# Optimization experiments

Hardware: AMD Instinct MI355X
Metric: run time of the kernel (lower is better)

The kernel has to match this reference:

```python
import jax, jax.numpy as jnp
import numpy as np
import math

B, T, E, H, HS = 8, 2048, 384, 6, 64

def setup_inputs() -> dict:
    key = jax.random.key(0)
    ks = jax.random.split(key, 5)
    scale = 1.0 / math.sqrt(E)
    return {
        "x": jax.random.normal(ks[0], (B, T, E), dtype=jnp.float32),
        "Wq": jax.random.normal(ks[1], (H, E, HS), dtype=jnp.float32) * scale,
        "Wk": jax.random.normal(ks[2], (H, E, HS), dtype=jnp.float32) * scale,
        "Wv": jax.random.normal(ks[3], (H, E, HS), dtype=jnp.float32) * scale,
        "Wo": jax.random.normal(ks[4], (H, HS, E), dtype=jnp.float32) * (1.0 / math.sqrt(HS)),
    }

def reference(x, Wq, Wk, Wv, Wo):
    # x: [B,T,E]; per-head projections batched over heads.
    q = jnp.einsum('bte,hed->bhtd', x, Wq)  # [B,H,T,HS]
    k = jnp.einsum('bte,hed->bhtd', x, Wk)
    v = jnp.einsum('bte,hed->bhtd', x, Wv)
    scores = jnp.einsum('bhid,bhjd->bhij', q, k)  # [B,H,T,T]
    # Faithful to source: MULTIPLICATIVE tril mask (masked logits become 0, not -inf),
    # then scale by 1/sqrt(head_size), then softmax.
    t = x.shape[1]
    tril = jnp.tril(jnp.ones((t, t), dtype=scores.dtype))
    scores = scores * tril / math.sqrt(HS)
    attn = jax.nn.softmax(scores, axis=-1)
    ctx = jnp.einsum('bhij,bhjd->bhid', attn, v)  # [B,H,T,HS]
    # Per-head output projection to embed dim, summed over heads (source accumulates).
    out = jnp.einsum('bhtd,hde->bte', ctx, Wo)  # [B,T,E]
    return out
```

## Files before the change

### kernel.cpp

```cpp
#include <hip/hip_runtime.h>
#include <math.h>

#define BBATCH 8
#define TSEQ   2048
#define EDIM   384
#define NHEAD  6
#define DHEAD  64
#define NBH    48
#define QTILE  128
#define NQT    16
#define NW1    442368
#define NW2    147456
#define XSZ    6291456
#define KVSZ   6291456
#define NSLOT  40

typedef __attribute__((ext_vector_type(8)))  short bf16x8;
typedef __attribute__((ext_vector_type(16))) float f32x16;
typedef __attribute__((ext_vector_type(2)))  int   i32x2;
typedef unsigned short u16;
typedef unsigned int   u32;

#define MFMA(a, b, c) __builtin_amdgcn_mfma_f32_32x32x16_bf16(a, b, c, 0, 0, 0)

__device__ __forceinline__ u16 f2bf(float f) {
  u32 u = __float_as_uint(f);
  return (u16)((u + 0x7fffu + ((u >> 16) & 1u)) >> 16);
}
__device__ __forceinline__ float bf2f(u16 h) {
  return __uint_as_float(((u32)h) << 16);
}
__device__ __forceinline__ bf16x8 mk8(u32 w0, u32 w1, u32 w2, u32 w3) {
  union { u32 u[4]; bf16x8 v; } t;
  t.u[0] = w0; t.u[1] = w1; t.u[2] = w2; t.u[3] = w3;
  return t.v;
}

__device__ const unsigned char SLOT_QT[NSLOT] = {
  3,4,5,6,7,7,8,8,9,9,10,10,11,11,11,12,12,12,13,13,13,14,14,14,15,15,15,15,
  2,6,10,14, 1,5,9,13, 0,4,8,12};
__device__ const unsigned char SLOT_C[NSLOT] = {
  0,0,0,0,0,1,0,1,0,1,0,1,0,1,2,0,1,2,0,1,2,0,1,2,0,1,2,3,
  0,1,2,3, 0,1,2,3, 0,1,2,3};

__global__ __launch_bounds__(256) void prep_w_k(
    const float* __restrict__ Wq, const float* __restrict__ Wk,
    const float* __restrict__ Wv, const float* __restrict__ Wo,
    u16* __restrict__ wtH, u16* __restrict__ wtL,
    u16* __restrict__ woH, u16* __restrict__ woL) {
  int idx = blockIdx.x * 256 + threadIdx.x;
  if (idx < NW1) {
    int d = idx & 63;
    int q = idx >> 6;
    int e = q % EDIM;
    int ph = q / EDIM;
    const float* W = (ph < 6) ? Wq : (ph < 12) ? Wk : Wv;
    int h = ph % 6;
    float v = W[((size_t)h * EDIM + e) * DHEAD + d];
    u16 hi = f2bf(v);
    size_t o = ((size_t)ph * DHEAD + d) * EDIM + e;
    wtH[o] = hi;
    wtL[o] = f2bf(v - bf2f(hi));
  } else {
    int o = idx - NW1;
    int eo = o % EDIM;
    int hd = o / EDIM;
    float v = Wo[(size_t)hd * EDIM + eo];
    u16 hi = f2bf(v);
    size_t oo = (size_t)eo * EDIM + hd;
    woH[oo] = hi;
    woL[oo] = f2bf(v - bf2f(hi));
  }
}

__global__ __launch_bounds__(256) void splitx_k(
    const float* __restrict__ x, u16* __restrict__ xh, u16* __restrict__ xl) {
  int i = (blockIdx.x * 256 + threadIdx.x) * 8;
  float4 a = *(const float4*)(x + i);
  float4 b = *(const float4*)(x + i + 4);
  u16 h0 = f2bf(a.x), h1 = f2bf(a.y), h2 = f2bf(a.z), h3 = f2bf(a.w);
  u16 h4 = f2bf(b.x), h5 = f2bf(b.y), h6 = f2bf(b.z), h7 = f2bf(b.w);
  uint4 H, L;
  H.x = (u32)h0 | ((u32)h1 << 16); H.y = (u32)h2 | ((u32)h3 << 16);
  H.z = (u32)h4 | ((u32)h5 << 16); H.w = (u32)h6 | ((u32)h7 << 16);
  L.x = (u32)f2bf(a.x - bf2f(h0)) | ((u32)f2bf(a.y - bf2f(h1)) << 16);
  L.y = (u32)f2bf(a.z - bf2f(h2)) | ((u32)f2bf(a.w - bf2f(h3)) << 16);
  L.z = (u32)f2bf(b.x - bf2f(h4)) | ((u32)f2bf(b.y - bf2f(h5)) << 16);
  L.w = (u32)f2bf(b.z - bf2f(h6)) | ((u32)f2bf(b.w - bf2f(h7)) << 16);
  *(uint4*)(xh + i) = H;
  *(uint4*)(xl + i) = L;
}

__global__ __launch_bounds__(256, 2) void proj_k(
    const u16* __restrict__ xh, const u16* __restrict__ xl,
    const u16* __restrict__ wtH, const u16* __restrict__ wtL,
    u16* __restrict__ qh, u16* __restrict__ ql,
    u16* __restrict__ kh, u16* __restrict__ kl,
    u16* __restrict__ vTh, u16* __restrict__ vTl,
    float* __restrict__ psum) {
  __shared__ __align__(16) unsigned char sm[32768];
  const int tid = threadIdx.x;
  const int w = tid >> 6, l = tid & 63, lh = l >> 5, l31 = l & 31;
  const int gid = ((blockIdx.x & 7) * 288) + ((int)blockIdx.x >> 3);
  const int bx = gid / 18, ph = gid % 18;
  const int p = ph / 6, h = ph % 6;
  const int bt0 = bx * 128;
  const u16* __restrict__ wBh = wtH + (size_t)ph * DHEAD * EDIM;
  const u16* __restrict__ wBl = wtL + (size_t)ph * DHEAD * EDIM;

  f32x16 acc0, acc1;
#pragma unroll
  for (int i = 0; i < 16; ++i) { acc0[i] = 0.f; acc1[i] = 0.f; }

  for (int k0 = 0; k0 < EDIM; k0 += 64) {
    __syncthreads();
#pragma unroll
    for (int i = 0; i < 4; ++i) {
      int c = tid + i * 256;
      int r = c >> 3, s = c & 7;
      int off = (r * 128 + s * 16) ^ ((r & 7) << 4);
      size_t g = (size_t)(bt0 + r) * EDIM + k0 + s * 8;
      *(uint4*)(sm + off) = *(const uint4*)(xh + g);
      *(uint4*)(sm + 16384 + off) = *(const uint4*)(xl + g);
    }
    __syncthreads();
    const int arow = 32 * w + l31;
#pragma unroll
    for (int ks = 0; ks < 4; ++ks) {
      int aoff = (arow * 128 + ks * 32 + 16 * lh) ^ ((arow & 7) << 4);
      bf16x8 aH = *(const bf16x8*)(sm + aoff);
      bf16x8 aL = *(const bf16x8*)(sm + 16384 + aoff);
      int eoff = k0 + ks * 16 + 8 * lh;
      size_t b0 = (size_t)l31 * EDIM + eoff;
      size_t b1 = (size_t)(32 + l31) * EDIM + eoff;
      bf16x8 bH0 = *(const bf16x8*)(wBh + b0);
      bf16x8 bL0 = *(const bf16x8*)(wBl + b0);
      bf16x8 bH1 = *(const bf16x8*)(wBh + b1);
      bf16x8 bL1 = *(const bf16x8*)(wBl + b1);
      acc0 = MFMA(aH, bH0, acc0); acc0 = MFMA(aH, bL0, acc0); acc0 = MFMA(aL, bH0, acc0);
      acc1 = MFMA(aH, bH1, acc1); acc1 = MFMA(aH, bL1, acc1); acc1 = MFMA(aL, bH1, acc1);
    }
  }

  const int b = bt0 >> 11, t0b = bt0 & (TSEQ - 1);
  const int bh = b * NHEAD + h;
  const float scale = (p == 0) ? 0.125f : 1.0f;

  if (p < 2) {
    u16* oH = (p == 0) ? qh : kh;
    u16* oL = (p == 0) ? ql : kl;
#pragma unroll
    for (int reg = 0; reg < 16; ++reg) {
      int row = (reg & 3) + 8 * (reg >> 2) + 4 * lh + 32 * w;
      size_t base = ((size_t)bh * TSEQ + t0b + row) * DHEAD;
      float v0 = acc0[reg] * scale, v1 = acc1[reg] * scale;
      u16 h0 = f2bf(v0), h1 = f2bf(v1);
      oH[base + l31] = h0;       oL[base + l31] = f2bf(v0 - bf2f(h0));
      oH[base + 32 + l31] = h1;  oL[base + 32 + l31] = f2bf(v1 - bf2f(h1));
    }
  } else {
    u16* T = (u16*)sm;
#pragma unroll
    for (int half = 0; half < 2; ++half) {
      __syncthreads();
#pragma unroll
      for (int reg = 0; reg < 16; ++reg) {
        int t = (reg & 3) + 8 * (reg >> 2) + 4 * lh + 32 * w;
        float v0 = acc0[reg], v1 = acc1[reg];
        u16 e0, e1;
        if (half == 0) { e0 = f2bf(v0); e1 = f2bf(v1); }
        else {
          u16 a0 = f2bf(v0), a1 = f2bf(v1);
          e0 = f2bf(v0 - bf2f(a0)); e1 = f2bf(v1 - bf2f(a1));
        }
        T[l31 * 132 + t] = e0;
        T[(32 + l31) * 132 + t] = e1;
      }
      __syncthreads();
      u16* dst = half ? vTl : vTh;
#pragma unroll
      for (int i = 0; i < 8; ++i) {
        int c = tid + i * 256;
        int d = c >> 5, s = c & 31;
        uint2 val = *(const uint2*)(T + d * 132 + s * 4);
        *(uint2*)(dst + ((size_t)bh * DHEAD + d) * TSEQ + t0b + s * 4) = val;
      }
    }
    float s0 = 0.f, s1 = 0.f;
#pragma unroll
    for (int reg = 0; reg < 16; ++reg) { s0 += acc0[reg]; s1 += acc1[reg]; }
    s0 += __shfl_xor(s0, 32);
    s1 += __shfl_xor(s1, 32);
    __syncthreads();
    float* ps = (float*)sm;
    if (lh == 0) { ps[w * 64 + l31] = s0; ps[w * 64 + 32 + l31] = s1; }
    __syncthreads();
    if (tid < 64) {
      float t = ps[tid] + ps[64 + tid] + ps[128 + tid] + ps[192 + tid];
      int tile = t0b >> 7;
      psum[((size_t)bh * NQT + tile) * DHEAD + tid] = t;
    }
  }
}

__global__ __launch_bounds__(256, 4) void attn_k(
    const u16* __restrict__ qh, const u16* __restrict__ ql,
    const u16* __restrict__ kh, const u16* __restrict__ kl,
    const u16* __restrict__ vTh, const u16* __restrict__ vTl,
    float* __restrict__ pO, float* __restrict__ pl) {
  __shared__ __align__(16) unsigned char sm[32768];
  const int oKl = 8192, oVh = 16384, oVl = 24576;
  const int tid = threadIdx.x;
  const int w = tid >> 6, l = tid & 63, lh = l >> 5, l31 = l & 31;
  const int gid = ((blockIdx.x & 7) * 240) + ((int)blockIdx.x >> 3);
  const int bh = gid / NSLOT, slot = gid % NSLOT;
  const int qt = SLOT_QT[slot], cch = SLOT_C[slot];
  const int tbeg = cch * 8;
  const int tend = min(cch * 8 + 8, 2 * qt + 2);
  const int t0 = qt * QTILE;
  const size_t kvb = (size_t)bh * TSEQ * DHEAD;

#pragma unroll
  for (int i = 0; i < 4; ++i) {
    int c = tid + i * 256;
    int r = c >> 3, s = c & 7;
    int off = (r * 128 + s * 16) ^ ((r & 7) << 4);
    size_t g = kvb + (size_t)(t0 + r) * DHEAD + s * 8;
    *(uint4*)(sm + off) = *(const uint4*)(qh + g);
    *(uint4*)(sm + 16384 + off) = *(const uint4*)(ql + g);
  }
  __syncthreads();
  bf16x8 qfH[4], qfL[4];
  {
    const int qrow = 32 * w + l31;
#pragma unroll
    for (int ks = 0; ks < 4; ++ks) {
      int off = (qrow * 128 + ks * 32 + 16 * lh) ^ ((qrow & 7) << 4);
      qfH[ks] = *(const bf16x8*)(sm + off);
      qfL[ks] = *(const bf16x8*)(sm + 16384 + off);
    }
  }
  uint4 kpH[2], kpL[2], vpH[2], vpL[2];
#pragma unroll
  for (int i = 0; i < 2; ++i) {
    int c = tid + i * 256;
    int r = c >> 3, s = c & 7;
    int j0 = tbeg * 64;
    kpH[i] = *(const uint4*)(kh + kvb + (size_t)(j0 + r) * DHEAD + s * 8);
    kpL[i] = *(const uint4*)(kl + kvb + (size_t)(j0 + r) * DHEAD + s * 8);
    vpH[i] = *(const uint4*)(vTh + kvb + (size_t)r * TSEQ + j0 + s * 8);
    vpL[i] = *(const uint4*)(vTl + kvb + (size_t)r * TSEQ + j0 + s * 8);
  }
  __syncthreads();

  f32x16 accO0, accO1;
#pragma unroll
  for (int i = 0; i < 16; ++i) { accO0[i] = 0.f; accO1[i] = 0.f; }
  float lrun = 0.f;
  const int qg = t0 + 32 * w + l31;

  for (int jt = tbeg; jt < tend; ++jt) {
#pragma unroll
    for (int i = 0; i < 2; ++i) {
      int c = tid + i * 256;
      int r = c >> 3, s = c & 7;
      int off = (r * 128 + s * 16) ^ ((r & 7) << 4);
      *(uint4*)(sm + off) = kpH[i];
      *(uint4*)(sm + oKl + off) = kpL[i];
      *(uint4*)(sm + oVh + off) = vpH[i];
      *(uint4*)(sm + oVl + off) = vpL[i];
    }
    __syncthreads();
    if (jt + 1 < tend) {
      int j0 = (jt + 1) * 64;
#pragma unroll
      for (int i = 0; i < 2; ++i) {
        int c = tid + i * 256;
        int r = c >> 3, s = c & 7;
        kpH[i] = *(const uint4*)(kh + kvb + (size_t)(j0 + r) * DHEAD + s * 8);
        kpL[i] = *(const uint4*)(kl + kvb + (size_t)(j0 + r) * DHEAD + s * 8);
        vpH[i] = *(const uint4*)(vTh + kvb + (size_t)r * TSEQ + j0 + s * 8);
        vpL[i] = *(const uint4*)(vTl + kvb + (size_t)r * TSEQ + j0 + s * 8);
      }
    }
#pragma unroll
    for (int jh = 0; jh < 2; ++jh) {
      f32x16 accS;
#pragma unroll
      for (int i = 0; i < 16; ++i) accS[i] = 0.f;
      const int krow = jh * 32 + l31;
      const int ksw = (l31 & 7) << 4;
      __builtin_amdgcn_s_setprio(1);
#pragma unroll
      for (int ks = 0; ks < 4; ++ks) {
        int koff = (krow * 128 + ks * 32 + 16 * lh) ^ ksw;
        bf16x8 aH = *(const bf16x8*)(sm + koff);
        bf16x8 aL = *(const bf16x8*)(sm + oKl + koff);
        accS = MFMA(aH, qfH[ks], accS);
        accS = MFMA(aH, qfL[ks], accS);
        accS = MFMA(aL, qfH[ks], accS);
      }
      __builtin_amdgcn_s_setprio(0);
      const int jb = jt * 64 + jh * 32 + 4 * lh;
      float ps = 0.f;
#pragma unroll
      for (int ml = 0; ml < 2; ++ml) {
        int rb = ml * 8;
        u32 hw[4], lw[4];
#pragma unroll
        for (int pr = 0; pr < 4; ++pr) {
          int r0 = rb + 2 * pr;
          int jg0 = jb + (r0 & 3) + 8 * (r0 >> 2);
          float s0 = (jg0 > qg) ? 0.f : accS[r0];
          float s1 = ((jg0 + 1) > qg) ? 0.f : accS[r0 + 1];
          float p0 = __expf(s0), p1 = __expf(s1);
          ps += p0 + p1;
          u16 a0 = f2bf(p0), a1 = f2bf(p1);
          hw[pr] = (u32)a0 | ((u32)a1 << 16);
          lw[pr] = (u32)f2bf(p0 - bf2f(a0)) | ((u32)f2bf(p1 - bf2f(a1)) << 16);
        }
        i32x2 s1 = __builtin_amdgcn_permlane32_swap((int)hw[0], (int)hw[2], false, false);
        i32x2 s2 = __builtin_amdgcn_permlane32_swap((int)hw[1], (int)hw[3], false, false);
        bf16x8 pH = mk8((u32)s1.x, (u32)s2.x, (u32)s1.y, (u32)s2.y);
        i32x2 t1 = __builtin_amdgcn_permlane32_swap((int)lw[0], (int)lw[2], false, false);
        i32x2 t2 = __builtin_amdgcn_permlane32_swap((int)lw[1], (int)lw[3], false, false);
        bf16x8 pL = mk8((u32)t1.x, (u32)t2.x, (u32)t1.y, (u32)t2.y);
        int m = jh * 2 + ml;
        int vo0 = (l31 * 128 + m * 32 + 16 * lh) ^ ksw;
        int vo1 = ((32 + l31) * 128 + m * 32 + 16 * lh) ^ ksw;
        bf16x8 vH0 = *(const bf16x8*)(sm + oVh + vo0);
        bf16x8 vL0 = *(const bf16x8*)(sm + oVl + vo0);
        bf16x8 vH1 = *(const bf16x8*)(sm + oVh + vo1);
        bf16x8 vL1 = *(const bf16x8*)(sm + oVl + vo1);
        __builtin_amdgcn_s_setprio(1);
        accO0 = MFMA(pH, vH0, accO0); accO0 = MFMA(pH, vL0, accO0); accO0 = MFMA(pL, vH0, accO0);
        accO1 = MFMA(pH, vH1, accO1); accO1 = MFMA(pH, vL1, accO1); accO1 = MFMA(pL, vH1, accO1);
        __builtin_amdgcn_s_setprio(0);
      }
      lrun += ps;
    }
    __syncthreads();
  }

  lrun += __shfl_xor(lrun, 32);
  const size_t slotO = ((size_t)bh * NQT + qt);
  if (lh == 0)
    atomicAdd(&pl[slotO * 128 + 32 * w + l31], lrun);
  float* po = pO + slotO * 8192;
#pragma unroll
  for (int reg = 0; reg < 16; ++reg) {
    int r = (reg & 3) + 8 * (reg >> 2) + 4 * lh + 32 * w;
    atomicAdd(&po[r * 64 + l31], accO0[reg]);
    atomicAdd(&po[r * 64 + 32 + l31], accO1[reg]);
  }
}

__global__ __launch_bounds__(256) void combine_k(
    const float* __restrict__ pO, const float* __restrict__ pl,
    const float* __restrict__ psum,
    u16* __restrict__ cxh, u16* __restrict__ cxl) {
  const int bid = blockIdx.x;
  const int bh = bid >> 4, qt = bid & 15;
  const int b = bh / NHEAD, h = bh % NHEAD;
  const int tid = threadIdx.x;
  const int d = tid & 63, rg = tid >> 6;
  float tail = 0.f;
  for (int tt = qt + 1; tt < NQT; ++tt)
    tail += psum[((size_t)bh * NQT + tt) * DHEAD + d];
  const float tcnt = (float)(TSEQ - (qt + 1) * 128);
  const float* po = pO + (size_t)bid * 8192;
  const float* plp = pl + (size_t)bid * 128;
#pragma unroll 4
  for (int k = 0; k < 32; ++k) {
    int r = rg * 32 + k;
    float inv = 1.0f / (plp[r] + tcnt);
    float v = (po[r * 64 + d] + tail) * inv;
    u16 hbits = f2bf(v);
    size_t o = ((size_t)b * TSEQ + qt * 128 + r) * EDIM + h * DHEAD + d;
    cxh[o] = hbits;
    cxl[o] = f2bf(v - bf2f(hbits));
  }
}

__global__ __launch_bounds__(256, 2) void outproj_k(
    const u16* __restrict__ cxh, const u16* __restrict__ cxl,
    const u16* __restrict__ woH, const u16* __restrict__ woL,
    float* __restrict__ out) {
  __shared__ __align__(16) unsigned char sm[32768];
  const int tid = threadIdx.x;
  const int w = tid >> 6, l = tid & 63, lh = l >> 5, l31 = l & 31;
  const int gid = ((blockIdx.x & 7) * 96) + ((int)blockIdx.x >> 3);
  const int bx = gid / 6, ey = gid % 6;
  const int bt0 = bx * 128, e0 = ey * 64;

  f32x16 acc0, acc1;
#pragma unroll
  for (int i = 0; i < 16; ++i) { acc0[i] = 0.f; acc1[i] = 0.f; }

  for (int k0 = 0; k0 < EDIM; k0 += 64) {
    __syncthreads();
#pragma unroll
    for (int i = 0; i < 4; ++i) {
      int c = tid + i * 256;
      int r = c >> 3, s = c & 7;
      int off = (r * 128 + s * 16) ^ ((r & 7) << 4);
      size_t g = (size_t)(bt0 + r) * EDIM + k0 + s * 8;
      *(uint4*)(sm + off) = *(const uint4*)(cxh + g);
      *(uint4*)(sm + 16384 + off) = *(const uint4*)(cxl + g);
    }
    __syncthreads();
    const int arow = 32 * w + l31;
#pragma unroll
    for (int ks = 0; ks < 4; ++ks) {
      int aoff = (arow * 128 + ks * 32 + 16 * lh) ^ ((arow & 7) << 4);
      bf16x8 aH = *(const bf16x8*)(sm + aoff);
      bf16x8 aL = *(const bf16x8*)(sm + 16384 + aoff);
      int hdoff = k0 + ks * 16 + 8 * lh;
      size_t b0 = (size_t)(e0 + l31) * EDIM + hdoff;
      size_t b1 = (size_t)(e0 + 32 + l31) * EDIM + hdoff;
      bf16x8 bH0 = *(const bf16x8*)(woH + b0);
      bf16x8 bL0 = *(const bf16x8*)(woL + b0);
      bf16x8 bH1 = *(const bf16x8*)(woH + b1);
      bf16x8 bL1 = *(const bf16x8*)(woL + b1);
      acc0 = MFMA(aH, bH0, acc0); acc0 = MFMA(aH, bL0, acc0); acc0 = MFMA(aL, bH0, acc0);
      acc1 = MFMA(aH, bH1, acc1); acc1 = MFMA(aH, bL1, acc1); acc1 = MFMA(aL, bH1, acc1);
    }
  }
#pragma unroll
  for (int reg = 0; reg < 16; ++reg) {
    int row = (reg & 3) + 8 * (reg >> 2) + 4 * lh + 32 * w;
    size_t o = (size_t)(bt0 + row) * EDIM + e0;
    out[o + l31] = acc0[reg];
    out[o + 32 + l31] = acc1[reg];
  }
}

extern "C" void kernel_launch(void* const* d_in, const int* in_sizes, int n_in,
                              void* d_out, int out_size, void* d_ws, size_t ws_size,
                              hipStream_t stream) {
  (void)in_sizes; (void)n_in; (void)out_size; (void)ws_size;
  const float* x  = (const float*)d_in[0];
  const float* Wq = (const float*)d_in[1];
  const float* Wk = (const float*)d_in[2];
  const float* Wv = (const float*)d_in[3];
  const float* Wo = (const float*)d_in[4];
  float* out = (float*)d_out;

  u16* qh  = (u16*)d_ws;
  u16* ql  = qh + KVSZ;
  u16* kh  = ql + KVSZ;
  u16* kl  = kh + KVSZ;
  u16* vTh = kl + KVSZ;
  u16* vTl = vTh + KVSZ;
  u16* xh  = vTl + KVSZ;
  u16* xl  = xh + XSZ;
  u16* wtH = xl + XSZ;
  u16* wtL = wtH + NW1;
  u16* woH = wtL + NW1;
  u16* woL = woH + NW2;
  float* psum = (float*)(woL + NW2);
  float* pO   = psum + (size_t)NBH * NQT * DHEAD;
  float* pl   = pO + (size_t)NBH * NQT * 128 * 64;
  u16* cxh = xh;
  u16* cxl = xl;

  hipMemsetAsync(pO, 0, ((size_t)NBH * NQT * 128 * 65) * sizeof(float), stream);
  hipLaunchKernelGGL(prep_w_k, dim3((NW1 + NW2) / 256), dim3(256), 0, stream,
                     Wq, Wk, Wv, Wo, wtH, wtL, woH, woL);
  hipLaunchKernelGGL(splitx_k, dim3(XSZ / 2048), dim3(256), 0, stream, x, xh, xl);
  hipLaunchKernelGGL(proj_k, dim3(2304), dim3(256), 0, stream,
                     xh, xl, wtH, wtL, qh, ql, kh, kl, vTh, vTl, psum);
  hipLaunchKernelGGL(attn_k, dim3(1920), dim3(256), 0, stream,
                     qh, ql, kh, kl, vTh, vTl, pO, pl);
  hipLaunchKernelGGL(combine_k, dim3(NBH * NQT), dim3(256), 0, stream,
                     pO, pl, psum, cxh, cxl);
  hipLaunchKernelGGL(outproj_k, dim3(768), dim3(256), 0, stream,
                     cxh, cxl, woH, woL, out);
}
```

Before: 551.2 us.

## Use single-wave attention blocks reading K/V from global, fuse combine step

The attention kernel is restructured from 256-thread blocks with LDS-staged K/V and split-KV slots into 64-thread single-wave blocks. Each block owns 32 query rows and walks the whole causal key range, loading K and V fragments straight from global memory (relying on cache). The softmax normalisation and masked-tail correction now happen in the epilogue, so the separate combine kernel, the atomics and the memset are removed. The QK accumulation is also split over two accumulators to shorten MFMA dependency chains. The cost is heavier per-wave global/L2 traffic for K/V with no LDS sharing, and causal load imbalance because work is no longer split across KV chunks.

Result: faster. 460.6 us (-16.4%).

```diff
diff --git a/kernel.cpp b/kernel.cpp
--- a/kernel.cpp
+++ b/kernel.cpp
@@ -13,7 +13,6 @@
 #define NW2    147456
 #define XSZ    6291456
 #define KVSZ   6291456
-#define NSLOT  40
 
 typedef __attribute__((ext_vector_type(8)))  short bf16x8;
 typedef __attribute__((ext_vector_type(16))) float f32x16;
@@ -35,13 +34,6 @@
   t.u[0] = w0; t.u[1] = w1; t.u[2] = w2; t.u[3] = w3;
   return t.v;
 }
-
-__device__ const unsigned char SLOT_QT[NSLOT] = {
-  3,4,5,6,7,7,8,8,9,9,10,10,11,11,11,12,12,12,13,13,13,14,14,14,15,15,15,15,
-  2,6,10,14, 1,5,9,13, 0,4,8,12};
-__device__ const unsigned char SLOT_C[NSLOT] = {
-  0,0,0,0,0,1,0,1,0,1,0,1,0,1,2,0,1,2,0,1,2,0,1,2,0,1,2,3,
-  0,1,2,3, 0,1,2,3, 0,1,2,3};
 
 __global__ __launch_bounds__(256) void prep_w_k(
     const float* __restrict__ Wq, const float* __restrict__ Wk,
@@ -203,104 +195,62 @@
   }
 }
 
-__global__ __launch_bounds__(256, 4) void attn_k(
+__global__ __launch_bounds__(64, 3) void attn_k(
     const u16* __restrict__ qh, const u16* __restrict__ ql,
     const u16* __restrict__ kh, const u16* __restrict__ kl,
     const u16* __restrict__ vTh, const u16* __restrict__ vTl,
-    float* __restrict__ pO, float* __restrict__ pl) {
-  __shared__ __align__(16) unsigned char sm[32768];
-  const int oKl = 8192, oVh = 16384, oVl = 24576;
-  const int tid = threadIdx.x;
-  const int w = tid >> 6, l = tid & 63, lh = l >> 5, l31 = l & 31;
-  const int gid = ((blockIdx.x & 7) * 240) + ((int)blockIdx.x >> 3);
-  const int bh = gid / NSLOT, slot = gid % NSLOT;
-  const int qt = SLOT_QT[slot], cch = SLOT_C[slot];
-  const int tbeg = cch * 8;
-  const int tend = min(cch * 8 + 8, 2 * qt + 2);
+    const float* __restrict__ psum,
+    u16* __restrict__ cxh, u16* __restrict__ cxl) {
+  const int l = threadIdx.x;
+  const int lh = l >> 5, l31 = l & 31;
+  const int xcd = blockIdx.x & 7;
+  const int idx = (int)blockIdx.x >> 3;
+  const int qt = (NQT - 1) - (idx / 24);
+  const int rem = idx % 24;
+  const int bhl = rem >> 2, ws = rem & 3;
+  const int bh = xcd * 6 + bhl;
+  const int b = bh / NHEAD, h = bh % NHEAD;
   const int t0 = qt * QTILE;
   const size_t kvb = (size_t)bh * TSEQ * DHEAD;
 
-#pragma unroll
-  for (int i = 0; i < 4; ++i) {
-    int c = tid + i * 256;
-    int r = c >> 3, s = c & 7;
-    int off = (r * 128 + s * 16) ^ ((r & 7) << 4);
-    size_t g = kvb + (size_t)(t0 + r) * DHEAD + s * 8;
-    *(uint4*)(sm + off) = *(const uint4*)(qh + g);
-    *(uint4*)(sm + 16384 + off) = *(const uint4*)(ql + g);
-  }
-  __syncthreads();
+  const int qglo = t0 + 32 * ws;
   bf16x8 qfH[4], qfL[4];
-  {
-    const int qrow = 32 * w + l31;
-#pragma unroll
-    for (int ks = 0; ks < 4; ++ks) {
-      int off = (qrow * 128 + ks * 32 + 16 * lh) ^ ((qrow & 7) << 4);
-      qfH[ks] = *(const bf16x8*)(sm + off);
-      qfL[ks] = *(const bf16x8*)(sm + 16384 + off);
-    }
-  }
-  uint4 kpH[2], kpL[2], vpH[2], vpL[2];
-#pragma unroll
-  for (int i = 0; i < 2; ++i) {
-    int c = tid + i * 256;
-    int r = c >> 3, s = c & 7;
-    int j0 = tbeg * 64;
-    kpH[i] = *(const uint4*)(kh + kvb + (size_t)(j0 + r) * DHEAD + s * 8);
-    kpL[i] = *(const uint4*)(kl + kvb + (size_t)(j0 + r) * DHEAD + s * 8);
-    vpH[i] = *(const uint4*)(vTh + kvb + (size_t)r * TSEQ + j0 + s * 8);
-    vpL[i] = *(const uint4*)(vTl + kvb + (size_t)r * TSEQ + j0 + s * 8);
-  }
-  __syncthreads();
+#pragma unroll
+  for (int ks = 0; ks < 4; ++ks) {
+    size_t g = kvb + (size_t)(qglo + l31) * DHEAD + ks * 16 + 8 * lh;
+    qfH[ks] = *(const bf16x8*)(qh + g);
+    qfL[ks] = *(const bf16x8*)(ql + g);
+  }
 
   f32x16 accO0, accO1;
 #pragma unroll
   for (int i = 0; i < 16; ++i) { accO0[i] = 0.f; accO1[i] = 0.f; }
   float lrun = 0.f;
-  const int qg = t0 + 32 * w + l31;
-
-  for (int jt = tbeg; jt < tend; ++jt) {
-#pragma unroll
-    for (int i = 0; i < 2; ++i) {
-      int c = tid + i * 256;
-      int r = c >> 3, s = c & 7;
-      int off = (r * 128 + s * 16) ^ ((r & 7) << 4);
-      *(uint4*)(sm + off) = kpH[i];
-      *(uint4*)(sm + oKl + off) = kpL[i];
-      *(uint4*)(sm + oVh + off) = vpH[i];
-      *(uint4*)(sm + oVl + off) = vpL[i];
-    }
-    __syncthreads();
-    if (jt + 1 < tend) {
-      int j0 = (jt + 1) * 64;
-#pragma unroll
-      for (int i = 0; i < 2; ++i) {
-        int c = tid + i * 256;
-        int r = c >> 3, s = c & 7;
-        kpH[i] = *(const uint4*)(kh + kvb + (size_t)(j0 + r) * DHEAD + s * 8);
-        kpL[i] = *(const uint4*)(kl + kvb + (size_t)(j0 + r) * DHEAD + s * 8);
-        vpH[i] = *(const uint4*)(vTh + kvb + (size_t)r * TSEQ + j0 + s * 8);
-        vpL[i] = *(const uint4*)(vTl + kvb + (size_t)r * TSEQ + j0 + s * 8);
-      }
-    }
+  const int qg = qglo + l31;
+  const int S = 2 * (qt + 1);
+
+  for (int jt = 0; jt < S; ++jt) {
 #pragma unroll
     for (int jh = 0; jh < 2; ++jh) {
-      f32x16 accS;
-#pragma unroll
-      for (int i = 0; i < 16; ++i) accS[i] = 0.f;
-      const int krow = jh * 32 + l31;
-      const int ksw = (l31 & 7) << 4;
+      f32x16 accSa, accSb;
+#pragma unroll
+      for (int i = 0; i < 16; ++i) { accSa[i] = 0.f; accSb[i] = 0.f; }
+      const size_t krow = kvb + (size_t)(jt * 64 + jh * 32 + l31) * DHEAD;
       __builtin_amdgcn_s_setprio(1);
 #pragma unroll
       for (int ks = 0; ks < 4; ++ks) {
-        int koff = (krow * 128 + ks * 32 + 16 * lh) ^ ksw;
-        bf16x8 aH = *(const bf16x8*)(sm + koff);
-        bf16x8 aL = *(const bf16x8*)(sm + oKl + koff);
-        accS = MFMA(aH, qfH[ks], accS);
-        accS = MFMA(aH, qfL[ks], accS);
-        accS = MFMA(aL, qfH[ks], accS);
+        size_t g = krow + ks * 16 + 8 * lh;
+        bf16x8 aH = *(const bf16x8*)(kh + g);
+        bf16x8 aL = *(const bf16x8*)(kl + g);
+        accSa = MFMA(aH, qfH[ks], accSa);
+        accSb = MFMA(aH, qfL[ks], accSb);
+        accSb = MFMA(aL, qfH[ks], accSb);
       }
       __builtin_amdgcn_s_setprio(0);
+      f32x16 accS;
+#pragma unroll
+      for (int i = 0; i < 16; ++i) accS[i] = accSa[i] + accSb[i];
+
       const int jb = jt * 64 + jh * 32 + 4 * lh;
       float ps = 0.f;
 #pragma unroll
@@ -326,12 +276,13 @@
         i32x2 t2 = __builtin_amdgcn_permlane32_swap((int)lw[1], (int)lw[3], false, false);
         bf16x8 pL = mk8((u32)t1.x, (u32)t2.x, (u32)t1.y, (u32)t2.y);
         int m = jh * 2 + ml;
-        int vo0 = (l31 * 128 + m * 32 + 16 * lh) ^ ksw;
-        int vo1 = ((32 + l31) * 128 + m * 32 + 16 * lh) ^ ksw;
-        bf16x8 vH0 = *(const bf16x8*)(sm + oVh + vo0);
-        bf16x8 vL0 = *(const bf16x8*)(sm + oVl + vo0);
-        bf16x8 vH1 = *(const bf16x8*)(sm + oVh + vo1);
-        bf16x8 vL1 = *(const bf16x8*)(sm + oVl + vo1);
+        size_t vcol = (size_t)jt * 64 + m * 16 + 8 * lh;
+        size_t v0 = kvb + (size_t)l31 * TSEQ + vcol;
+        size_t v1 = kvb + (size_t)(32 + l31) * TSEQ + vcol;
+        bf16x8 vH0 = *(const bf16x8*)(vTh + v0);
+        bf16x8 vL0 = *(const bf16x8*)(vTl + v0);
+        bf16x8 vH1 = *(const bf16x8*)(vTh + v1);
+        bf16x8 vL1 = *(const bf16x8*)(vTl + v1);
         __builtin_amdgcn_s_setprio(1);
         accO0 = MFMA(pH, vH0, accO0); accO0 = MFMA(pH, vL0, accO0); accO0 = MFMA(pL, vH0, accO0);
         accO1 = MFMA(pH, vH1, accO1); accO1 = MFMA(pH, vL1, accO1); accO1 = MFMA(pL, vH1, accO1);
@@ -339,46 +290,31 @@
       }
       lrun += ps;
     }
-    __syncthreads();
   }
 
   lrun += __shfl_xor(lrun, 32);
-  const size_t slotO = ((size_t)bh * NQT + qt);
-  if (lh == 0)
-    atomicAdd(&pl[slotO * 128 + 32 * w + l31], lrun);
-  float* po = pO + slotO * 8192;
+  lrun += (float)(TSEQ - S * 64);
+  {
+    float tl0 = 0.f, tl1 = 0.f;
+    for (int tt = qt + 1; tt < NQT; ++tt) {
+      const float* ps = psum + ((size_t)bh * NQT + tt) * DHEAD;
+      tl0 += ps[l31];
+      tl1 += ps[32 + l31];
+    }
+#pragma unroll
+    for (int reg = 0; reg < 16; ++reg) { accO0[reg] += tl0; accO1[reg] += tl1; }
+  }
 #pragma unroll
   for (int reg = 0; reg < 16; ++reg) {
-    int r = (reg & 3) + 8 * (reg >> 2) + 4 * lh + 32 * w;
-    atomicAdd(&po[r * 64 + l31], accO0[reg]);
-    atomicAdd(&po[r * 64 + 32 + l31], accO1[reg]);
-  }
-}
-
-__global__ __launch_bounds__(256) void combine_k(
-    const float* __restrict__ pO, const float* __restrict__ pl,
-    const float* __restrict__ psum,
-    u16* __restrict__ cxh, u16* __restrict__ cxl) {
-  const int bid = blockIdx.x;
-  const int bh = bid >> 4, qt = bid & 15;
-  const int b = bh / NHEAD, h = bh % NHEAD;
-  const int tid = threadIdx.x;
-  const int d = tid & 63, rg = tid >> 6;
-  float tail = 0.f;
-  for (int tt = qt + 1; tt < NQT; ++tt)
-    tail += psum[((size_t)bh * NQT + tt) * DHEAD + d];
-  const float tcnt = (float)(TSEQ - (qt + 1) * 128);
-  const float* po = pO + (size_t)bid * 8192;
-  const float* plp = pl + (size_t)bid * 128;
-#pragma unroll 4
-  for (int k = 0; k < 32; ++k) {
-    int r = rg * 32 + k;
-    float inv = 1.0f / (plp[r] + tcnt);
-    float v = (po[r * 64 + d] + tail) * inv;
-    u16 hbits = f2bf(v);
-    size_t o = ((size_t)b * TSEQ + qt * 128 + r) * EDIM + h * DHEAD + d;
-    cxh[o] = hbits;
-    cxl[o] = f2bf(v - bf2f(hbits));
+    int qrow = (reg & 3) + 8 * (reg >> 2) + 4 * lh;
+    float lq = __shfl(lrun, qrow);
+    float inv = 1.f / lq;
+    int t = qglo + qrow;
+    size_t o = ((size_t)b * TSEQ + t) * EDIM + h * DHEAD;
+    float v0 = accO0[reg] * inv, v1 = accO1[reg] * inv;
+    u16 h0 = f2bf(v0), h1 = f2bf(v1);
+    cxh[o + l31] = h0;       cxl[o + l31] = f2bf(v0 - bf2f(h0));
+    cxh[o + 32 + l31] = h1;  cxl[o + 32 + l31] = f2bf(v1 - bf2f(h1));
   }
 }
 
@@ -459,21 +395,16 @@
   u16* woH = wtL + NW1;
   u16* woL = woH + NW2;
   float* psum = (float*)(woL + NW2);
-  float* pO   = psum + (size_t)NBH * NQT * DHEAD;
-  float* pl   = pO + (size_t)NBH * NQT * 128 * 64;
   u16* cxh = xh;
   u16* cxl = xl;
 
-  hipMemsetAsync(pO, 0, ((size_t)NBH * NQT * 128 * 65) * sizeof(float), stream);
   hipLaunchKernelGGL(prep_w_k, dim3((NW1 + NW2) / 256), dim3(256), 0, stream,
                      Wq, Wk, Wv, Wo, wtH, wtL, woH, woL);
   hipLaunchKernelGGL(splitx_k, dim3(XSZ / 2048), dim3(256), 0, stream, x, xh, xl);
   hipLaunchKernelGGL(proj_k, dim3(2304), dim3(256), 0, stream,
                      xh, xl, wtH, wtL, qh, ql, kh, kl, vTh, vTl, psum);
-  hipLaunchKernelGGL(attn_k, dim3(1920), dim3(256), 0, stream,
-                     qh, ql, kh, kl, vTh, vTl, pO, pl);
-  hipLaunchKernelGGL(combine_k, dim3(NBH * NQT), dim3(256), 0, stream,
-                     pO, pl, psum, cxh, cxl);
+  hipLaunchKernelGGL(attn_k, dim3(3072), dim3(64), 0, stream,
+                     qh, ql, kh, kl, vTh, vTl, psum, cxh, cxl);
   hipLaunchKernelGGL(outproj_k, dim3(768), dim3(256), 0, stream,
                      cxh, cxl, woH, woL, out);
 }
```
